# Performance work log

Measured on AMD Instinct MI355X. Metric: run time of the kernel, lower is better.

The kernel has to match this reference:

```python
import jax, jax.numpy as jnp
import numpy as np

NUM_HEADS = 4
HEAD_DIM = 64
BN_EPS = 1e-5


def setup_inputs() -> dict:
    key = jax.random.key(0)
    ks = jax.random.split(key, 6)
    B, C, H, W = 8, 256, 48, 48
    HD = NUM_HEADS * HEAD_DIM  # 256
    x = jax.random.normal(ks[0], (B, C, H, W), dtype=jnp.float32)
    q_w = jax.random.normal(ks[1], (HD, C), dtype=jnp.float32) * (1.0 / np.sqrt(C))
    k_w = jax.random.normal(ks[2], (HEAD_DIM, C), dtype=jnp.float32) * (1.0 / np.sqrt(C))
    v_w = jax.random.normal(ks[3], (HEAD_DIM, C), dtype=jnp.float32) * (1.0 / np.sqrt(C))
    proj_w = jax.random.normal(ks[4], (C, HD), dtype=jnp.float32) * (1.0 / np.sqrt(HD))
    proj_b = jnp.zeros((C,), dtype=jnp.float32)
    gamma = jnp.ones((C,), dtype=jnp.float32)
    beta = jnp.zeros((C,), dtype=jnp.float32)
    return {"x": x, "q_w": q_w, "k_w": k_w, "v_w": v_w,
            "proj_w": proj_w, "proj_b": proj_b, "gamma": gamma, "beta": beta}


def reference(x, q_w, k_w, v_w, proj_w, proj_b, gamma, beta):
    B, C, H, W = x.shape
    N = H * W
    scale = HEAD_DIM ** -0.5
    xf = x.reshape(B, C, N)  # 1x1 conv == channel matmul
    q = jnp.einsum('oc,bcn->bon', q_w, xf).reshape(B, NUM_HEADS, HEAD_DIM, N)
    k = jnp.einsum('dc,bcn->bdn', k_w, xf)  # shared single KV head (MQA)
    v = jnp.einsum('dc,bcn->bdn', v_w, xf)
    # scores: [B, heads, N, N]
    attn = jnp.einsum('bhdn,bdm->bhnm', q, k) * scale
    attn = jax.nn.softmax(attn, axis=-1)
    out = jnp.einsum('bhnm,bdm->bhdn', attn, v)  # [B, heads, d, N]
    out = out.reshape(B, NUM_HEADS * HEAD_DIM, N)
    out = jnp.einsum('co,bon->bcn', proj_w, out) + proj_b[None, :, None]
    out = out.reshape(B, C, H, W)
    # BatchNorm2d (training-mode batch statistics, biased variance)
    mean = jnp.mean(out, axis=(0, 2, 3), keepdims=True)
    var = jnp.var(out, axis=(0, 2, 3), keepdims=True)
    out = gamma[None, :, None, None] * (out - mean) * jax.lax.rsqrt(var + BN_EPS) + beta[None, :, None, None]
    return out + x
```

## Files before the change

kernel.cpp:

```cpp
#include <hip/hip_runtime.h>
#include <hip/hip_bf16.h>
#include <math.h>

#define BB 8
#define CCH 256
#define NN 2304
#define NH 4
#define HDIM 64
#define QKV_ROWS 384
#define BN_EPS 1e-5f
#define NTILES 36
#define HTILES 18
#define NPART 288
#define SLOG2E 0.18033688011112042f

typedef short bf16x8 __attribute__((ext_vector_type(8)));
typedef short bf16x4 __attribute__((ext_vector_type(4)));
typedef float f32x4 __attribute__((ext_vector_type(4)));

#if __has_builtin(__builtin_amdgcn_exp2f)
#define EXP2(x) __builtin_amdgcn_exp2f(x)
#else
#define EXP2(x) __expf((x) * 0.6931471805599453f)
#endif

#define MFMA16(a, b, c) __builtin_amdgcn_mfma_f32_16x16x16bf16_1k(a, b, c, 0, 0, 0)
#define MFMA32(a, b, c) __builtin_amdgcn_mfma_f32_16x16x32_bf16(a, b, c, 0, 0, 0)

__device__ __forceinline__ unsigned bfpair(float a, float b) {
    __hip_bfloat162 h = __float22bfloat162_rn(make_float2(a, b));
    return *(unsigned*)&h;
}
__device__ __forceinline__ unsigned short f2bf(float f) {
    unsigned u = __float_as_uint(f);
    u = (u + 0x7FFFu + ((u >> 16) & 1u)) >> 16;
    return (unsigned short)u;
}
__device__ __forceinline__ bf16x4 pack4(float p0, float p1, float p2, float p3) {
    union { unsigned u[2]; bf16x4 v; } x;
    x.u[0] = bfpair(p0, p1);
    x.u[1] = bfpair(p2, p3);
    return x.v;
}
__device__ __forceinline__ float bf2f(unsigned short s) {
    return __uint_as_float((unsigned)s << 16);
}

__global__ __launch_bounds__(256) void prep_k(
    const float* __restrict__ x,
    const float* __restrict__ qw, const float* __restrict__ kw,
    const float* __restrict__ vw, const float* __restrict__ pw,
    unsigned short* __restrict__ xT, unsigned short* __restrict__ xb,
    unsigned short* __restrict__ Wb, unsigned short* __restrict__ Pb)
{
    const int bid = blockIdx.x;
    const int tid = threadIdx.x;
    if (bid < 1152) {
        __shared__ float sX[64][65];
        const int b  = bid / 144;
        const int rem = bid - b * 144;
        const int nb = (rem >> 2) * 64;
        const int cb = (rem & 3) * 64;

        #pragma unroll
        for (int u = 0; u < 4; ++u) {
            int c  = (tid >> 4) + 16 * u;
            int n4 = (tid & 15) * 4;
            float4 v = *(const float4*)(x + ((size_t)(b * CCH + cb + c)) * NN + nb + n4);
            sX[c][n4+0] = v.x; sX[c][n4+1] = v.y; sX[c][n4+2] = v.z; sX[c][n4+3] = v.w;
        }
        __syncthreads();

        const int n  = tid >> 2;
        const int cg = (tid & 3) * 16;
        unsigned vals[8];
        #pragma unroll
        for (int p = 0; p < 8; ++p)
            vals[p] = bfpair(sX[cg + 2*p][n], sX[cg + 2*p + 1][n]);
        unsigned short* dst = xT + ((size_t)(b * NN + nb + n)) * CCH + cb + cg;
        *(uint4*)dst = make_uint4(vals[0], vals[1], vals[2], vals[3]);
        *(uint4*)(dst + 8) = make_uint4(vals[4], vals[5], vals[6], vals[7]);

        #pragma unroll
        for (int it = 0; it < 2; ++it) {
            int flat = tid + 256 * it;
            int row = flat >> 3;
            int n8  = (flat & 7) * 8;
            unsigned vv[4];
            #pragma unroll
            for (int p = 0; p < 4; ++p)
                vv[p] = bfpair(sX[row][n8 + 2*p], sX[row][n8 + 2*p + 1]);
            *(uint4*)(xb + ((size_t)(b * CCH + cb + row)) * NN + nb + n8) =
                make_uint4(vv[0], vv[1], vv[2], vv[3]);
        }
    } else {
        int idx = (bid - 1152) * 256 + tid;
        if (idx < 98304) {
            int o = idx >> 8, c = idx & 255;
            float v;
            if (o < 256)      v = qw[(size_t)o * CCH + c] * SLOG2E;
            else if (o < 320) v = kw[(size_t)(o - 256) * CCH + c];
            else              v = vw[(size_t)(o - 320) * CCH + c];
            Wb[idx] = f2bf(v);
        } else {
            int j = idx - 98304;
            if (j < 65536) Pb[j] = f2bf(pw[j]);
        }
    }
}

__global__ __launch_bounds__(128) void qkv_mfma_k(
    const unsigned short* __restrict__ Wb, const unsigned short* __restrict__ xT,
    unsigned short* __restrict__ Qt, unsigned short* __restrict__ Kt,
    unsigned short* __restrict__ Vn)
{
    __shared__ unsigned short sE[2][64 * 72];
    const int tid = threadIdx.x;
    const int wave = tid >> 6;
    const int lane = tid & 63;
    const int quad = lane >> 4;
    const int l15  = lane & 15;
    const int b  = blockIdx.x;
    const int nb = blockIdx.y * 64;
    const int mb = blockIdx.z * 128 + wave * 64;

    const unsigned short* Ab = Wb + (size_t)(mb + l15) * CCH + quad * 8;
    const unsigned short* Bb = xT + ((size_t)(b * NN + nb + l15)) * CCH + quad * 8;

    f32x4 C[4][4] = {};
    bf16x8 aA[2][4], bB[2][4];
    #pragma unroll
    for (int i = 0; i < 4; ++i) aA[0][i] = *(const bf16x8*)(Ab + (size_t)(16*i) * CCH);
    #pragma unroll
    for (int j = 0; j < 4; ++j) bB[0][j] = *(const bf16x8*)(Bb + (size_t)(16*j) * CCH);

    #pragma unroll
    for (int kk = 0; kk < 8; ++kk) {
        const int cur = kk & 1;
        if (kk < 7) {
            const int k1 = (kk + 1) * 32;
            #pragma unroll
            for (int i = 0; i < 4; ++i) aA[cur^1][i] = *(const bf16x8*)(Ab + (size_t)(16*i) * CCH + k1);
            #pragma unroll
            for (int j = 0; j < 4; ++j) bB[cur^1][j] = *(const bf16x8*)(Bb + (size_t)(16*j) * CCH + k1);
        }
        #pragma unroll
        for (int i = 0; i < 4; ++i)
            #pragma unroll
            for (int j = 0; j < 4; ++j)
                C[i][j] = MFMA32(aA[cur][i], bB[cur][j], C[i][j]);
    }

    unsigned short* sEw = &sE[wave][0];
    if (mb < 320) {
        #pragma unroll
        for (int i = 0; i < 4; ++i)
            #pragma unroll
            for (int j = 0; j < 4; ++j) {
                unsigned p01 = bfpair(C[i][j][0], C[i][j][1]);
                unsigned p23 = bfpair(C[i][j][2], C[i][j][3]);
                unsigned short* p = sEw + (16*j + l15) * 72 + 16*i + quad*4;
                *(unsigned*)p = p01;
                *(unsigned*)(p + 2) = p23;
            }
        if (mb < 256) {
            #pragma unroll
            for (int it = 0; it < 8; ++it) {
                int flat = lane + 64 * it;
                int row = flat >> 3;
                int o8  = (flat & 7) * 8;
                uint4 v = *(const uint4*)(sEw + row * 72 + o8);
                *(uint4*)(Qt + ((size_t)(b * NN + nb + row)) * CCH + mb + o8) = v;
            }
        } else {
            #pragma unroll
            for (int it = 0; it < 8; ++it) {
                int flat = lane + 64 * it;
                int row = flat >> 3;
                int o8  = (flat & 7) * 8;
                uint4 v = *(const uint4*)(sEw + row * 72 + o8);
                *(uint4*)(Kt + ((size_t)(b * NN + nb + row)) * 64 + o8) = v;
            }
        }
    } else {
        #pragma unroll
        for (int i = 0; i < 4; ++i)
            #pragma unroll
            for (int j = 0; j < 4; ++j) {
                unsigned p01 = bfpair(C[i][j][0], C[i][j][1]);
                unsigned p23 = bfpair(C[i][j][2], C[i][j][3]);
                unsigned short* p = sEw + (16*i + quad*4) * 72 + 16*j + l15;
                p[0]   = (unsigned short)p01;
                p[72]  = (unsigned short)(p01 >> 16);
                p[144] = (unsigned short)p23;
                p[216] = (unsigned short)(p23 >> 16);
            }
        #pragma unroll
        for (int it = 0; it < 8; ++it) {
            int flat = lane + 64 * it;
            int row = flat >> 3;
            int n8  = (flat & 7) * 8;
            uint4 v = *(const uint4*)(sEw + row * 72 + n8);
            *(uint4*)(Vn + ((size_t)(b * 64 + (mb - 320) + row)) * NN + nb + n8) = v;
        }
    }
}

__global__ __launch_bounds__(512, 4) void attn_k(
    const unsigned short* __restrict__ Qt,
    const unsigned short* __restrict__ Kt,
    const unsigned short* __restrict__ Vn,
    unsigned short* __restrict__ Ao)
{
    __shared__ __align__(16) unsigned short sKV[4 * 64 * 72];

    const int tid   = threadIdx.x;
    const int wave  = tid >> 6;
    const int lane  = tid & 63;
    const int quad  = lane >> 4;
    const int l15   = lane & 15;
    const int qslot = wave & 1;
    const int kh    = (wave >> 1) & 1;
    const int hloc  = wave >> 2;
    const int qoff  = qslot * 32;
    const int b     = blockIdx.x;
    const int nb    = blockIdx.y * 64;
    const int head  = blockIdx.z * 2 + hloc;

    unsigned short* sKb = sKV + kh * 2 * 4608;
    unsigned short* sVb = sKb + 4608;

    const bf16x4 vone = {(short)0x3F80, (short)0x3F80, (short)0x3F80, (short)0x3F80};

    bf16x8 bQ[2][2];
    const unsigned short* QtB = Qt + ((size_t)(b * NN + nb + qoff + l15)) * CCH + head * 64 + quad * 8;
    #pragma unroll
    for (int qt = 0; qt < 2; ++qt)
        #pragma unroll
        for (int s = 0; s < 2; ++s)
            bQ[qt][s] = *(const bf16x8*)(QtB + (size_t)(16*qt) * CCH + s * 32);

    const int srow = tid >> 3;
    const int sch8 = (tid & 7) * 8;
    bf16x8 pf[4];
    #pragma unroll
    for (int u = 0; u < 4; ++u) {
        const int keys0 = (u >> 1) * HTILES * 64;
        if ((u & 1) == 0)
            pf[u] = *(const bf16x8*)(Kt + ((size_t)(b * NN + keys0 + srow)) * 64 + sch8);
        else
            pf[u] = *(const bf16x8*)(Vn + ((size_t)(b * 64 + srow)) * NN + keys0 + sch8);
    }

    f32x4 O[4][2] = {};
    f32x4 dacc[2] = {};

    for (int step = 0; step < HTILES; ++step) {
        __syncthreads();
        #pragma unroll
        for (int u = 0; u < 4; ++u)
            *(bf16x8*)(sKV + u * 4608 + srow * 72 + sch8) = pf[u];
        __syncthreads();

        if (step + 1 < HTILES) {
            #pragma unroll
            for (int u = 0; u < 4; ++u) {
                const int keys0 = ((u >> 1) * HTILES + step + 1) * 64;
                if ((u & 1) == 0)
                    pf[u] = *(const bf16x8*)(Kt + ((size_t)(b * NN + keys0 + srow)) * 64 + sch8);
                else
                    pf[u] = *(const bf16x8*)(Vn + ((size_t)(b * 64 + srow)) * NN + keys0 + sch8);
            }
        }

        f32x4 C[4][2] = {};
        #pragma unroll
        for (int s = 0; s < 2; ++s)
            #pragma unroll
            for (int kt = 0; kt < 4; ++kt) {
                bf16x8 aK = *(const bf16x8*)(sKb + (16*kt + l15) * 72 + s * 32 + quad * 8);
                C[kt][0] = MFMA32(aK, bQ[0][s], C[kt][0]);
                C[kt][1] = MFMA32(aK, bQ[1][s], C[kt][1]);
            }

        bf16x4 bP[4][2];
        #pragma unroll
        for (int kt = 0; kt < 4; ++kt)
            #pragma unroll
            for (int qt = 0; qt < 2; ++qt)
                bP[kt][qt] = pack4(EXP2(C[kt][qt][0]), EXP2(C[kt][qt][1]),
                                   EXP2(C[kt][qt][2]), EXP2(C[kt][qt][3]));

        #pragma unroll
        for (int kt = 0; kt < 4; ++kt) {
            dacc[0] = MFMA16(vone, bP[kt][0], dacc[0]);
            dacc[1] = MFMA16(vone, bP[kt][1], dacc[1]);
        }

        #pragma unroll
        for (int jd = 0; jd < 4; ++jd)
            #pragma unroll
            for (int kt = 0; kt < 4; ++kt) {
                bf16x4 aV = *(const bf16x4*)(sVb + (16*jd + l15) * 72 + 16*kt + quad*4);
                O[jd][0] = MFMA16(aV, bP[kt][0], O[jd][0]);
                O[jd][1] = MFMA16(aV, bP[kt][1], O[jd][1]);
            }
    }
    __syncthreads();

    float* sc = (float*)sKV;
    const int base = (hloc * 2 + qslot) * 2304 + lane * 36;
    if (kh == 1) {
        #pragma unroll
        for (int jd = 0; jd < 4; ++jd)
            #pragma unroll
            for (int qt = 0; qt < 2; ++qt)
                *(f32x4*)(sc + base + jd * 8 + qt * 4) = O[jd][qt];
        sc[base + 32] = dacc[0][0];
        sc[base + 33] = dacc[1][0];
    }
    __syncthreads();
    float rinv[2] = {0.f, 0.f};
    if (kh == 0) {
        #pragma unroll
        for (int jd = 0; jd < 4; ++jd)
            #pragma unroll
            for (int qt = 0; qt < 2; ++qt)
                O[jd][qt] += *(const f32x4*)(sc + base + jd * 8 + qt * 4);
        rinv[0] = 1.0f / (dacc[0][0] + sc[base + 32]);
        rinv[1] = 1.0f / (dacc[1][0] + sc[base + 33]);
    }
    __syncthreads();

    unsigned short* sT = (unsigned short*)sKV;
    if (kh == 0) {
        #pragma unroll
        for (int qt = 0; qt < 2; ++qt)
            #pragma unroll
            for (int jd = 0; jd < 4; ++jd) {
                unsigned lo = bfpair(O[jd][qt][0] * rinv[qt], O[jd][qt][1] * rinv[qt]);
                unsigned hi = bfpair(O[jd][qt][2] * rinv[qt], O[jd][qt][3] * rinv[qt]);
                *(uint2*)(sT + (hloc * 64 + qoff + 16*qt + l15) * 72 + 16*jd + quad*4) = make_uint2(lo, hi);
            }
    }
    __syncthreads();

    #pragma unroll
    for (int it = 0; it < 2; ++it) {
        int flat = tid + 512 * it;
        int hh   = flat >> 9;
        int row  = (flat >> 3) & 63;
        int c8   = (flat & 7) * 8;
        uint4 v = *(const uint4*)(sT + (hh * 64 + row) * 72 + c8);
        *(uint4*)(Ao + ((size_t)(b * NN + nb + row)) * CCH + (blockIdx.z * 2 + hh) * 64 + c8) = v;
    }
}

__global__ __launch_bounds__(128) void proj_mfma_k(
    const unsigned short* __restrict__ Pb, const unsigned short* __restrict__ Ao,
    const float* __restrict__ pb, unsigned short* __restrict__ projb,
    float* __restrict__ psum, float* __restrict__ psq)
{
    __shared__ unsigned short sE[2][64 * 72];
    const int tid = threadIdx.x;
    const int wave = tid >> 6;
    const int lane = tid & 63;
    const int quad = lane >> 4;
    const int l15  = lane & 15;
    const int b  = blockIdx.x;
    const int nb = blockIdx.y * 64;
    const int mb = blockIdx.z * 128 + wave * 64;
    const int part = b * NTILES + blockIdx.y;

    const unsigned short* Ab = Pb + (size_t)(mb + l15) * CCH + quad * 8;
    const unsigned short* Bb = Ao + ((size_t)(b * NN + nb + l15)) * CCH + quad * 8;

    f32x4 C[4][4] = {};
    bf16x8 aA[2][4], bB[2][4];
    #pragma unroll
    for (int i = 0; i < 4; ++i) aA[0][i] = *(const bf16x8*)(Ab + (size_t)(16*i) * CCH);
    #pragma unroll
    for (int j = 0; j < 4; ++j) bB[0][j] = *(const bf16x8*)(Bb + (size_t)(16*j) * CCH);

    #pragma unroll
    for (int kk = 0; kk < 8; ++kk) {
        const int cur = kk & 1;
        if (kk < 7) {
            const int k1 = (kk + 1) * 32;
            #pragma unroll
            for (int i = 0; i < 4; ++i) aA[cur^1][i] = *(const bf16x8*)(Ab + (size_t)(16*i) * CCH + k1);
            #pragma unroll
            for (int j = 0; j < 4; ++j) bB[cur^1][j] = *(const bf16x8*)(Bb + (size_t)(16*j) * CCH + k1);
        }
        #pragma unroll
        for (int i = 0; i < 4; ++i)
            #pragma unroll
            for (int j = 0; j < 4; ++j)
                C[i][j] = MFMA32(aA[cur][i], bB[cur][j], C[i][j]);
    }

    unsigned short* sEw = &sE[wave][0];
    #pragma unroll
    for (int i = 0; i < 4; ++i) {
        #pragma unroll
        for (int r = 0; r < 4; ++r) {
            const int ch = mb + 16*i + quad*4 + r;
            const float bias = pb[ch];
            float v0 = C[i][0][r] + bias, v1 = C[i][1][r] + bias;
            float v2 = C[i][2][r] + bias, v3 = C[i][3][r] + bias;
            C[i][0][r] = v0; C[i][1][r] = v1; C[i][2][r] = v2; C[i][3][r] = v3;
            float rs = (v0 + v1) + (v2 + v3);
            float rq = (v0*v0 + v1*v1) + (v2*v2 + v3*v3);
            rs += __shfl_xor(rs, 1); rq += __shfl_xor(rq, 1);
            rs += __shfl_xor(rs, 2); rq += __shfl_xor(rq, 2);
            rs += __shfl_xor(rs, 4); rq += __shfl_xor(rq, 4);
            rs += __shfl_xor(rs, 8); rq += __shfl_xor(rq, 8);
            if (l15 == 0) {
                psum[(size_t)ch * NPART + part] = rs;
                psq [(size_t)ch * NPART + part] = rq;
            }
        }
    }

    #pragma unroll
    for (int i = 0; i < 4; ++i)
        #pragma unroll
        for (int j = 0; j < 4; ++j) {
            unsigned p01 = bfpair(C[i][j][0], C[i][j][1]);
            unsigned p23 = bfpair(C[i][j][2], C[i][j][3]);
            unsigned short* p = sEw + (16*i + quad*4) * 72 + 16*j + l15;
            p[0]   = (unsigned short)p01;
            p[72]  = (unsigned short)(p01 >> 16);
            p[144] = (unsigned short)p23;
            p[216] = (unsigned short)(p23 >> 16);
        }
    #pragma unroll
    for (int it = 0; it < 8; ++it) {
        int flat = lane + 64 * it;
        int row = flat >> 3;
        int n8  = (flat & 7) * 8;
        uint4 v = *(const uint4*)(sEw + row * 72 + n8);
        *(uint4*)(projb + ((size_t)(b * CCH + mb + row)) * NN + nb + n8) = v;
    }
}

__global__ __launch_bounds__(256) void bn_apply_k(
    const unsigned short* __restrict__ projb, const unsigned short* __restrict__ xb,
    const float* __restrict__ psum, const float* __restrict__ psq,
    const float* __restrict__ gamma, const float* __restrict__ beta,
    float* __restrict__ out)
{
    const int tid = threadIdx.x;
    const int b = blockIdx.x;
    const int c = blockIdx.y;

    float s = 0.f, q = 0.f;
    for (int k = tid; k < NPART; k += 256) {
        s += psum[(size_t)c * NPART + k];
        q += psq [(size_t)c * NPART + k];
    }
    __shared__ float rs[256], rq[256];
    rs[tid] = s; rq[tid] = q;
    __syncthreads();
    for (int off = 128; off > 0; off >>= 1) {
        if (tid < off) { rs[tid] += rs[tid + off]; rq[tid] += rq[tid + off]; }
        __syncthreads();
    }
    const float inv_n = 1.0f / (float)(BB * NN);
    float mean = rs[0] * inv_n;
    float var  = rq[0] * inv_n - mean * mean;
    float scv = gamma[c] * rsqrtf(var + BN_EPS);
    float shv = beta[c] - mean * scv;

    #pragma unroll
    for (int it = 0; it < 2; ++it) {
        int chunk = tid + 256 * it;
        if (chunk < 288) {
            size_t base = ((size_t)(b * CCH + c)) * NN + chunk * 8;
            uint4 pv = *(const uint4*)(projb + base);
            uint4 xv = *(const uint4*)(xb + base);
            const unsigned short* pp = (const unsigned short*)&pv;
            const unsigned short* xx = (const unsigned short*)&xv;
            float4 r0, r1;
            r0.x = scv * bf2f(pp[0]) + shv + bf2f(xx[0]);
            r0.y = scv * bf2f(pp[1]) + shv + bf2f(xx[1]);
            r0.z = scv * bf2f(pp[2]) + shv + bf2f(xx[2]);
            r0.w = scv * bf2f(pp[3]) + shv + bf2f(xx[3]);
            r1.x = scv * bf2f(pp[4]) + shv + bf2f(xx[4]);
            r1.y = scv * bf2f(pp[5]) + shv + bf2f(xx[5]);
            r1.z = scv * bf2f(pp[6]) + shv + bf2f(xx[6]);
            r1.w = scv * bf2f(pp[7]) + shv + bf2f(xx[7]);
            *(float4*)(out + base) = r0;
            *(float4*)(out + base + 4) = r1;
        }
    }
}

extern "C" void kernel_launch(void* const* d_in, const int* in_sizes, int n_in,
                              void* d_out, int out_size, void* d_ws, size_t ws_size,
                              hipStream_t stream)
{
    const float* x     = (const float*)d_in[0];
    const float* qw    = (const float*)d_in[1];
    const float* kw    = (const float*)d_in[2];
    const float* vw    = (const float*)d_in[3];
    const float* pw    = (const float*)d_in[4];
    const float* pb    = (const float*)d_in[5];
    const float* gamma = (const float*)d_in[6];
    const float* beta  = (const float*)d_in[7];
    float* out = (float*)d_out;

    char* ws = (char*)d_ws;
    unsigned short* xT = (unsigned short*)ws;
    unsigned short* Ao = (unsigned short*)ws;
    unsigned short* Wb = (unsigned short*)(ws + 9437184);
    unsigned short* Pb = (unsigned short*)(ws + 9633792);
    unsigned short* Qt = (unsigned short*)(ws + 9764864);
    unsigned short* Kt = (unsigned short*)(ws + 19202048);
    unsigned short* Vn = (unsigned short*)(ws + 21561344);
    unsigned short* projb = (unsigned short*)(ws + 9764864);
    float* psum  = (float*)(ws + 28639232);
    float* psq   = (float*)(ws + 28934144);
    unsigned short* xb = (unsigned short*)(ws + 29229056);

    prep_k<<<1792, 256, 0, stream>>>(x, qw, kw, vw, pw, xT, xb, Wb, Pb);

    dim3 g1(BB, NN / 64, 3);
    qkv_mfma_k<<<g1, 128, 0, stream>>>(Wb, xT, Qt, Kt, Vn);

    dim3 g2(BB, NN / 64, NH / 2);
    attn_k<<<g2, 512, 0, stream>>>(Qt, Kt, Vn, Ao);

    dim3 g3(BB, NN / 64, 2);
    proj_mfma_k<<<g3, 128, 0, stream>>>(Pb, Ao, pb, projb, psum, psq);

    dim3 g4(BB, CCH);
    bn_apply_k<<<g4, 256, 0, stream>>>(projb, xb, psum, psq, gamma, beta, out);
}
```

Before: 200.8 us.

## Fuse x transpose/bf16 conversion into QKV projection kernel via shared memory

Removes the separate global xT transpose buffer: the QKV kernel now loads fp32 x tiles itself, converts them to bf16, writes xb for the residual, and keeps the transposed tile in LDS as the MFMA B operand. Each block now computes all 384 output rows with 6 waves instead of splitting across three z-blocks, so x is read once per tile instead of three times and the xT write/read round trip goes away. Weight conversion moves to its own small kernel. The trade-off is fewer, larger blocks (288 blocks of 384 threads) using about 52KB of LDS, which lowers occupancy, and an epilogue serialized into two rounds with extra barriers.

```diff
diff --git a/kernel.cpp b/kernel.cpp
--- a/kernel.cpp
+++ b/kernel.cpp
@@ -12,6 +12,7 @@
 #define NTILES 36
 #define HTILES 18
 #define NPART 288
+#define XP 280
 #define SLOG2E 0.18033688011112042f
 
 typedef short bf16x8 __attribute__((ext_vector_type(8)));
@@ -46,75 +47,36 @@
     return __uint_as_float((unsigned)s << 16);
 }
 
-__global__ __launch_bounds__(256) void prep_k(
-    const float* __restrict__ x,
+__global__ __launch_bounds__(256) void prep_w_k(
     const float* __restrict__ qw, const float* __restrict__ kw,
     const float* __restrict__ vw, const float* __restrict__ pw,
-    unsigned short* __restrict__ xT, unsigned short* __restrict__ xb,
     unsigned short* __restrict__ Wb, unsigned short* __restrict__ Pb)
 {
-    const int bid = blockIdx.x;
-    const int tid = threadIdx.x;
-    if (bid < 1152) {
-        __shared__ float sX[64][65];
-        const int b  = bid / 144;
-        const int rem = bid - b * 144;
-        const int nb = (rem >> 2) * 64;
-        const int cb = (rem & 3) * 64;
-
-        #pragma unroll
-        for (int u = 0; u < 4; ++u) {
-            int c  = (tid >> 4) + 16 * u;
-            int n4 = (tid & 15) * 4;
-            float4 v = *(const float4*)(x + ((size_t)(b * CCH + cb + c)) * NN + nb + n4);
-            sX[c][n4+0] = v.x; sX[c][n4+1] = v.y; sX[c][n4+2] = v.z; sX[c][n4+3] = v.w;
-        }
-        __syncthreads();
-
-        const int n  = tid >> 2;
-        const int cg = (tid & 3) * 16;
-        unsigned vals[8];
-        #pragma unroll
-        for (int p = 0; p < 8; ++p)
-            vals[p] = bfpair(sX[cg + 2*p][n], sX[cg + 2*p + 1][n]);
-        unsigned short* dst = xT + ((size_t)(b * NN + nb + n)) * CCH + cb + cg;
-        *(uint4*)dst = make_uint4(vals[0], vals[1], vals[2], vals[3]);
-        *(uint4*)(dst + 8) = make_uint4(vals[4], vals[5], vals[6], vals[7]);
-
-        #pragma unroll
-        for (int it = 0; it < 2; ++it) {
-            int flat = tid + 256 * it;
-            int row = flat >> 3;
-            int n8  = (flat & 7) * 8;
-            unsigned vv[4];
-            #pragma unroll
-            for (int p = 0; p < 4; ++p)
-                vv[p] = bfpair(sX[row][n8 + 2*p], sX[row][n8 + 2*p + 1]);
-            *(uint4*)(xb + ((size_t)(b * CCH + cb + row)) * NN + nb + n8) =
-                make_uint4(vv[0], vv[1], vv[2], vv[3]);
-        }
+    int idx = blockIdx.x * 256 + threadIdx.x;
+    if (idx < 98304) {
+        int o = idx >> 8, c = idx & 255;
+        float v;
+        if (o < 256)      v = qw[(size_t)o * CCH + c] * SLOG2E;
+        else if (o < 320) v = kw[(size_t)(o - 256) * CCH + c];
+        else              v = vw[(size_t)(o - 320) * CCH + c];
+        Wb[idx] = f2bf(v);
     } else {
-        int idx = (bid - 1152) * 256 + tid;
-        if (idx < 98304) {
-            int o = idx >> 8, c = idx & 255;
-            float v;
-            if (o < 256)      v = qw[(size_t)o * CCH + c] * SLOG2E;
-            else if (o < 320) v = kw[(size_t)(o - 256) * CCH + c];
-            else              v = vw[(size_t)(o - 320) * CCH + c];
-            Wb[idx] = f2bf(v);
-        } else {
-            int j = idx - 98304;
-            if (j < 65536) Pb[j] = f2bf(pw[j]);
-        }
-    }
-}
-
-__global__ __launch_bounds__(128) void qkv_mfma_k(
-    const unsigned short* __restrict__ Wb, const unsigned short* __restrict__ xT,
+        int j = idx - 98304;
+        if (j < 65536) Pb[j] = f2bf(pw[j]);
+    }
+}
+
+__global__ __launch_bounds__(384) void qkv_fused_k(
+    const float* __restrict__ x, const unsigned short* __restrict__ Wb,
+    unsigned short* __restrict__ xb,
     unsigned short* __restrict__ Qt, unsigned short* __restrict__ Kt,
     unsigned short* __restrict__ Vn)
 {
-    __shared__ unsigned short sE[2][64 * 72];
+    __shared__ __align__(16) char smem[16896 + 64 * XP * 2];
+    float* sX = (float*)smem;
+    unsigned short* xTl = (unsigned short*)(smem + 16896);
+    unsigned short* sE  = (unsigned short*)smem;
+
     const int tid = threadIdx.x;
     const int wave = tid >> 6;
     const int lane = tid & 63;
@@ -122,17 +84,46 @@
     const int l15  = lane & 15;
     const int b  = blockIdx.x;
     const int nb = blockIdx.y * 64;
-    const int mb = blockIdx.z * 128 + wave * 64;
+    const int mb = wave * 64;
+
+    for (int cpass = 0; cpass < 4; ++cpass) {
+        const int cb = cpass * 64;
+        __syncthreads();
+        for (int chunk = tid; chunk < 1024; chunk += 384) {
+            int c  = chunk >> 4;
+            int n4 = (chunk & 15) * 4;
+            float4 v = *(const float4*)(x + ((size_t)(b * CCH + cb + c)) * NN + nb + n4);
+            sX[c * 66 + n4 + 0] = v.x; sX[c * 66 + n4 + 1] = v.y;
+            sX[c * 66 + n4 + 2] = v.z; sX[c * 66 + n4 + 3] = v.w;
+        }
+        __syncthreads();
+        for (int u = tid; u < 512; u += 384) {
+            int row = u >> 3;
+            int n8  = (u & 7) * 8;
+            unsigned vv[4];
+            #pragma unroll
+            for (int p = 0; p < 4; ++p)
+                vv[p] = bfpair(sX[row * 66 + n8 + 2*p], sX[row * 66 + n8 + 2*p + 1]);
+            *(uint4*)(xb + ((size_t)(b * CCH + cb + row)) * NN + nb + n8) =
+                make_uint4(vv[0], vv[1], vv[2], vv[3]);
+        }
+        for (int u = tid; u < 512; u += 384) {
+            int n = u >> 3;
+            int g = (u & 7) * 8;
+            unsigned vv[4];
+            #pragma unroll
+            for (int p = 0; p < 4; ++p)
+                vv[p] = bfpair(sX[(g + 2*p) * 66 + n], sX[(g + 2*p + 1) * 66 + n]);
+            *(uint4*)(xTl + n * XP + cb + g) = make_uint4(vv[0], vv[1], vv[2], vv[3]);
+        }
+    }
+    __syncthreads();
 
     const unsigned short* Ab = Wb + (size_t)(mb + l15) * CCH + quad * 8;
-    const unsigned short* Bb = xT + ((size_t)(b * NN + nb + l15)) * CCH + quad * 8;
-
     f32x4 C[4][4] = {};
-    bf16x8 aA[2][4], bB[2][4];
+    bf16x8 aA[2][4];
     #pragma unroll
     for (int i = 0; i < 4; ++i) aA[0][i] = *(const bf16x8*)(Ab + (size_t)(16*i) * CCH);
-    #pragma unroll
-    for (int j = 0; j < 4; ++j) bB[0][j] = *(const bf16x8*)(Bb + (size_t)(16*j) * CCH);
 
     #pragma unroll
     for (int kk = 0; kk < 8; ++kk) {
@@ -140,69 +131,80 @@
         if (kk < 7) {
             const int k1 = (kk + 1) * 32;
             #pragma unroll
-            for (int i = 0; i < 4; ++i) aA[cur^1][i] = *(const bf16x8*)(Ab + (size_t)(16*i) * CCH + k1);
-            #pragma unroll
-            for (int j = 0; j < 4; ++j) bB[cur^1][j] = *(const bf16x8*)(Bb + (size_t)(16*j) * CCH + k1);
-        }
+            for (int i = 0; i < 4; ++i)
+                aA[cur^1][i] = *(const bf16x8*)(Ab + (size_t)(16*i) * CCH + k1);
+        }
+        bf16x8 bB[4];
+        #pragma unroll
+        for (int j = 0; j < 4; ++j)
+            bB[j] = *(const bf16x8*)(xTl + (16*j + l15) * XP + kk * 32 + quad * 8);
         #pragma unroll
         for (int i = 0; i < 4; ++i)
             #pragma unroll
             for (int j = 0; j < 4; ++j)
-                C[i][j] = MFMA32(aA[cur][i], bB[cur][j], C[i][j]);
-    }
-
-    unsigned short* sEw = &sE[wave][0];
-    if (mb < 320) {
-        #pragma unroll
-        for (int i = 0; i < 4; ++i)
-            #pragma unroll
-            for (int j = 0; j < 4; ++j) {
-                unsigned p01 = bfpair(C[i][j][0], C[i][j][1]);
-                unsigned p23 = bfpair(C[i][j][2], C[i][j][3]);
-                unsigned short* p = sEw + (16*j + l15) * 72 + 16*i + quad*4;
-                *(unsigned*)p = p01;
-                *(unsigned*)(p + 2) = p23;
+                C[i][j] = MFMA32(aA[cur][i], bB[j], C[i][j]);
+    }
+
+    __syncthreads();
+
+    #pragma unroll
+    for (int round = 0; round < 2; ++round) {
+        if (wave >= round * 3 && wave < round * 3 + 3) {
+            unsigned short* sEw = sE + (wave - round * 3) * 4608;
+            if (mb < 320) {
+                #pragma unroll
+                for (int i = 0; i < 4; ++i)
+                    #pragma unroll
+                    for (int j = 0; j < 4; ++j) {
+                        unsigned p01 = bfpair(C[i][j][0], C[i][j][1]);
+                        unsigned p23 = bfpair(C[i][j][2], C[i][j][3]);
+                        unsigned short* p = sEw + (16*j + l15) * 72 + 16*i + quad*4;
+                        *(unsigned*)p = p01;
+                        *(unsigned*)(p + 2) = p23;
+                    }
+                if (mb < 256) {
+                    #pragma unroll
+                    for (int it = 0; it < 8; ++it) {
+                        int flat = lane + 64 * it;
+                        int row = flat >> 3;
+                        int o8  = (flat & 7) * 8;
+                        uint4 v = *(const uint4*)(sEw + row * 72 + o8);
+                        *(uint4*)(Qt + ((size_t)(b * NN + nb + row)) * CCH + mb + o8) = v;
+                    }
+                } else {
+                    #pragma unroll
+                    for (int it = 0; it < 8; ++it) {
+                        int flat = lane + 64 * it;
+                        int row = flat >> 3;
+                        int o8  = (flat & 7) * 8;
+                        uint4 v = *(const uint4*)(sEw + row * 72 + o8);
+                        *(uint4*)(Kt + ((size_t)(b * NN + nb + row)) * 64 + o8) = v;
+                    }
+                }
+            } else {
+                #pragma unroll
+                for (int i = 0; i < 4; ++i)
+                    #pragma unroll
+                    for (int j = 0; j < 4; ++j) {
+                        unsigned p01 = bfpair(C[i][j][0], C[i][j][1]);
+                        unsigned p23 = bfpair(C[i][j][2], C[i][j][3]);
+                        unsigned short* p = sEw + (16*i + quad*4) * 72 + 16*j + l15;
+                        p[0]   = (unsigned short)p01;
+                        p[72]  = (unsigned short)(p01 >> 16);
+                        p[144] = (unsigned short)p23;
+                        p[216] = (unsigned short)(p23 >> 16);
+                    }
+                #pragma unroll
+                for (int it = 0; it < 8; ++it) {
+                    int flat = lane + 64 * it;
+                    int row = flat >> 3;
+                    int n8  = (flat & 7) * 8;
+                    uint4 v = *(const uint4*)(sEw + row * 72 + n8);
+                    *(uint4*)(Vn + ((size_t)(b * 64 + row)) * NN + nb + n8) = v;
+                }
             }
-        if (mb < 256) {
-            #pragma unroll
-            for (int it = 0; it < 8; ++it) {
-                int flat = lane + 64 * it;
-                int row = flat >> 3;
-                int o8  = (flat & 7) * 8;
-                uint4 v = *(const uint4*)(sEw + row * 72 + o8);
-                *(uint4*)(Qt + ((size_t)(b * NN + nb + row)) * CCH + mb + o8) = v;
-            }
-        } else {
-            #pragma unroll
-            for (int it = 0; it < 8; ++it) {
-                int flat = lane + 64 * it;
-                int row = flat >> 3;
-                int o8  = (flat & 7) * 8;
-                uint4 v = *(const uint4*)(sEw + row * 72 + o8);
-                *(uint4*)(Kt + ((size_t)(b * NN + nb + row)) * 64 + o8) = v;
-            }
-        }
-    } else {
-        #pragma unroll
-        for (int i = 0; i < 4; ++i)
-            #pragma unroll
-            for (int j = 0; j < 4; ++j) {
-                unsigned p01 = bfpair(C[i][j][0], C[i][j][1]);
-                unsigned p23 = bfpair(C[i][j][2], C[i][j][3]);
-                unsigned short* p = sEw + (16*i + quad*4) * 72 + 16*j + l15;
-                p[0]   = (unsigned short)p01;
-                p[72]  = (unsigned short)(p01 >> 16);
-                p[144] = (unsigned short)p23;
-                p[216] = (unsigned short)(p23 >> 16);
-            }
-        #pragma unroll
-        for (int it = 0; it < 8; ++it) {
-            int flat = lane + 64 * it;
-            int row = flat >> 3;
-            int n8  = (flat & 7) * 8;
-            uint4 v = *(const uint4*)(sEw + row * 72 + n8);
-            *(uint4*)(Vn + ((size_t)(b * 64 + (mb - 320) + row)) * NN + nb + n8) = v;
-        }
+        }
+        __syncthreads();
     }
 }
 
@@ -511,7 +513,6 @@
     float* out = (float*)d_out;
 
     char* ws = (char*)d_ws;
-    unsigned short* xT = (unsigned short*)ws;
     unsigned short* Ao = (unsigned short*)ws;
     unsigned short* Wb = (unsigned short*)(ws + 9437184);
     unsigned short* Pb = (unsigned short*)(ws + 9633792);
@@ -523,10 +524,10 @@
     float* psq   = (float*)(ws + 28934144);
     unsigned short* xb = (unsigned short*)(ws + 29229056);
 
-    prep_k<<<1792, 256, 0, stream>>>(x, qw, kw, vw, pw, xT, xb, Wb, Pb);
-
-    dim3 g1(BB, NN / 64, 3);
-    qkv_mfma_k<<<g1, 128, 0, stream>>>(Wb, xT, Qt, Kt, Vn);
+    prep_w_k<<<640, 256, 0, stream>>>(qw, kw, vw, pw, Wb, Pb);
+
+    dim3 g1(BB, NN / 64);
+    qkv_fused_k<<<g1, 384, 0, stream>>>(x, Wb, xb, Qt, Kt, Vn);
 
     dim3 g2(BB, NN / 64, NH / 2);
     attn_k<<<g2, 512, 0, stream>>>(Qt, Kt, Vn, Ao);
```

Result: slower. 205.7 us (+2.4%).

## Double-buffer K/V shared tiles with XOR swizzle in attention kernel

Applied to the files above, without the earlier changes.

Replaces the single padded K/V shared-memory tile with two unpadded buffers, so each step writes the next tile into the alternate buffer while computing on the current one. This removes one of the two block barriers per step, and global prefetch now runs two steps ahead. Padding is replaced by an XOR swizzle on 16-byte chunks to avoid LDS bank conflicts. Shared memory grows from about 36 KB to 64 KB per block, which may limit blocks per CU and occupancy at launch_bounds(512,4).

```diff
diff --git a/kernel.cpp b/kernel.cpp
--- a/kernel.cpp
+++ b/kernel.cpp
@@ -212,7 +212,7 @@
     const unsigned short* __restrict__ Vn,
     unsigned short* __restrict__ Ao)
 {
-    __shared__ __align__(16) unsigned short sKV[4 * 64 * 72];
+    __shared__ __align__(16) unsigned short sKV[2 * 4 * 64 * 64];
 
     const int tid   = threadIdx.x;
     const int wave  = tid >> 6;
@@ -227,9 +227,6 @@
     const int nb    = blockIdx.y * 64;
     const int head  = blockIdx.z * 2 + hloc;
 
-    unsigned short* sKb = sKV + kh * 2 * 4608;
-    unsigned short* sVb = sKb + 4608;
-
     const bf16x4 vone = {(short)0x3F80, (short)0x3F80, (short)0x3F80, (short)0x3F80};
 
     bf16x8 bQ[2][2];
@@ -241,44 +238,64 @@
             bQ[qt][s] = *(const bf16x8*)(QtB + (size_t)(16*qt) * CCH + s * 32);
 
     const int srow = tid >> 3;
-    const int sch8 = (tid & 7) * 8;
+    const int swch = ((tid & 7) ^ (srow & 7)) * 8;
+    const int sgc8 = (tid & 7) * 8;
+
     bf16x8 pf[4];
     #pragma unroll
     for (int u = 0; u < 4; ++u) {
         const int keys0 = (u >> 1) * HTILES * 64;
         if ((u & 1) == 0)
-            pf[u] = *(const bf16x8*)(Kt + ((size_t)(b * NN + keys0 + srow)) * 64 + sch8);
+            pf[u] = *(const bf16x8*)(Kt + ((size_t)(b * NN + keys0 + srow)) * 64 + sgc8);
         else
-            pf[u] = *(const bf16x8*)(Vn + ((size_t)(b * 64 + srow)) * NN + keys0 + sch8);
+            pf[u] = *(const bf16x8*)(Vn + ((size_t)(b * 64 + srow)) * NN + keys0 + sgc8);
+    }
+    #pragma unroll
+    for (int u = 0; u < 4; ++u)
+        *(bf16x8*)(sKV + u * 4096 + srow * 64 + swch) = pf[u];
+    #pragma unroll
+    for (int u = 0; u < 4; ++u) {
+        const int keys0 = ((u >> 1) * HTILES + 1) * 64;
+        if ((u & 1) == 0)
+            pf[u] = *(const bf16x8*)(Kt + ((size_t)(b * NN + keys0 + srow)) * 64 + sgc8);
+        else
+            pf[u] = *(const bf16x8*)(Vn + ((size_t)(b * 64 + srow)) * NN + keys0 + sgc8);
     }
 
     f32x4 O[4][2] = {};
     f32x4 dacc[2] = {};
 
     for (int step = 0; step < HTILES; ++step) {
+        const int cur = step & 1;
         __syncthreads();
-        #pragma unroll
-        for (int u = 0; u < 4; ++u)
-            *(bf16x8*)(sKV + u * 4608 + srow * 72 + sch8) = pf[u];
-        __syncthreads();
 
         if (step + 1 < HTILES) {
             #pragma unroll
+            for (int u = 0; u < 4; ++u)
+                *(bf16x8*)(sKV + (cur ^ 1) * 16384 + u * 4096 + srow * 64 + swch) = pf[u];
+        }
+        if (step + 2 < HTILES) {
+            #pragma unroll
             for (int u = 0; u < 4; ++u) {
-                const int keys0 = ((u >> 1) * HTILES + step + 1) * 64;
+                const int keys0 = ((u >> 1) * HTILES + step + 2) * 64;
                 if ((u & 1) == 0)
-                    pf[u] = *(const bf16x8*)(Kt + ((size_t)(b * NN + keys0 + srow)) * 64 + sch8);
+                    pf[u] = *(const bf16x8*)(Kt + ((size_t)(b * NN + keys0 + srow)) * 64 + sgc8);
                 else
-                    pf[u] = *(const bf16x8*)(Vn + ((size_t)(b * 64 + srow)) * NN + keys0 + sch8);
-            }
-        }
+                    pf[u] = *(const bf16x8*)(Vn + ((size_t)(b * 64 + srow)) * NN + keys0 + sgc8);
+            }
+        }
+
+        const unsigned short* sKb = sKV + cur * 16384 + kh * 2 * 4096;
+        const unsigned short* sVb = sKb + 4096;
 
         f32x4 C[4][2] = {};
         #pragma unroll
         for (int s = 0; s < 2; ++s)
             #pragma unroll
             for (int kt = 0; kt < 4; ++kt) {
-                bf16x8 aK = *(const bf16x8*)(sKb + (16*kt + l15) * 72 + s * 32 + quad * 8);
+                const int row = 16*kt + l15;
+                const int chsw = ((s*4 + quad) ^ (row & 7)) * 8;
+                bf16x8 aK = *(const bf16x8*)(sKb + row * 64 + chsw);
                 C[kt][0] = MFMA32(aK, bQ[0][s], C[kt][0]);
                 C[kt][1] = MFMA32(aK, bQ[1][s], C[kt][1]);
             }
@@ -301,7 +318,9 @@
         for (int jd = 0; jd < 4; ++jd)
             #pragma unroll
             for (int kt = 0; kt < 4; ++kt) {
-                bf16x4 aV = *(const bf16x4*)(sVb + (16*jd + l15) * 72 + 16*kt + quad*4);
+                const int row = 16*jd + l15;
+                const int chsw = ((2*kt + (quad >> 1)) ^ (row & 7)) * 8 + (quad & 1) * 4;
+                bf16x4 aV = *(const bf16x4*)(sVb + row * 64 + chsw);
                 O[jd][0] = MFMA16(aV, bP[kt][0], O[jd][0]);
                 O[jd][1] = MFMA16(aV, bP[kt][1], O[jd][1]);
             }
```

After: 199.1 us (median of 2 runs). About the same (-0.8%).
